# Kernel optimization log

Hardware: AMD Instinct MI355X
Metric: run time of the kernel (lower is better)

Reference implementation:

```python
import jax, jax.numpy as jnp
import numpy as np

SCALE = 2
BN_EPS = 1e-5


def setup_inputs() -> dict:
    key = jax.random.key(0)
    ks = jax.random.split(key, 12)
    B, C, H, W = 16, 256, 64, 64
    inter = C // 32  # reduce_ratio_nl = 32 -> 8
    f = lambda k, shape, s=0.05: jax.random.normal(k, shape, dtype=jnp.float32) * s
    return {
        "x": jax.random.normal(ks[0], (B, C, H, W), dtype=jnp.float32),
        "Wq": f(ks[1], (inter, C)), "bq": f(ks[2], (inter,)),
        "Wk": f(ks[3], (inter, C)), "bk": f(ks[4], (inter,)),
        "Wv": f(ks[5], (C, C)),    "bv": f(ks[6], (C,)),
        "gamma_nl": f(ks[7], (1,), 0.5),
        "convW": f(ks[8], (C, C, 3, 3)), "convb": f(ks[9], (C,)),
        "bn_w": jnp.ones((C,), jnp.float32),
        "bn_b": jnp.zeros((C,), jnp.float32),
        "bn_mean": f(ks[10], (C,)),
        "bn_var": jnp.ones((C,), jnp.float32),
        "gamma": f(ks[11], (1,), 0.5),
    }


def reference(x, Wq, bq, Wk, bk, Wv, bv, gamma_nl, convW, convb,
              bn_w, bn_b, bn_mean, bn_var, gamma):
    B, C, H, W = x.shape
    s = SCALE
    hb, wb = H // s, W // s
    L = hb * wb
    # split into s*s spatial blocks, batch them: [s*s*B, C, L]
    xb = (x.reshape(B, C, s, hb, s, wb)
           .transpose(2, 4, 0, 1, 3, 5)
           .reshape(s * s * B, C, L))
    # 1x1 conv projections == channel matmuls
    q = jnp.einsum('dc,ncl->ndl', Wq, xb) + bq[:, None]   # [N, d, L]
    k = jnp.einsum('dc,ncl->ndl', Wk, xb) + bk[:, None]
    v = jnp.einsum('dc,ncl->ndl', Wv, xb) + bv[:, None]   # [N, C, L]
    # energy[n,l,m] = sum_d q[n,d,l] * k[n,d,m]; softmax over last axis
    attn = jax.nn.softmax(jnp.einsum('ndl,ndm->nlm', q, k), axis=-1)
    # out[n,c,i] = sum_j v[n,c,j] * attn[n,i,j]
    out = jnp.einsum('ncj,nij->nci', v, attn)
    out = gamma_nl * out + xb
    # reassemble blocks -> [B, C, H, W]
    ctx = (out.reshape(s, s, B, C, hb, wb)
              .transpose(2, 3, 0, 4, 1, 5)
              .reshape(B, C, H, W))
    # 3x3 conv + BN (eval) + gamma-residual + ReLU
    y = jax.lax.conv_general_dilated(
        ctx, convW, window_strides=(1, 1), padding='SAME',
        dimension_numbers=('NCHW', 'OIHW', 'NCHW')) + convb[None, :, None, None]
    inv = (bn_w / jnp.sqrt(bn_var + BN_EPS))[None, :, None, None]
    y = (y - bn_mean[None, :, None, None]) * inv + bn_b[None, :, None, None]
    return jax.nn.relu(gamma * y + x)
```

## Files before the change

### kernel.cpp

```cpp
#include <hip/hip_runtime.h>
#include <hip/hip_bf16.h>
#include <math.h>

#define B_   16
#define C_   256
#define H_   64
#define W_   64
#define L_   1024
#define N_   64
#define D_   8

typedef _Float16 f16x8 __attribute__((ext_vector_type(8)));
typedef float    f32x4 __attribute__((ext_vector_type(4)));

static __device__ __forceinline__ unsigned short f16bits(float v) {
    _Float16 h = (_Float16)v;
    return *reinterpret_cast<unsigned short*>(&h);
}
static __device__ __forceinline__ float f16tof(unsigned short b) {
    _Float16 h = *reinterpret_cast<_Float16*>(&b);
    return (float)h;
}

__global__ __launch_bounds__(256) void qk_proj(
    const float* __restrict__ x, const float* __restrict__ Wq,
    const float* __restrict__ bq, const float* __restrict__ Wk,
    const float* __restrict__ bk, float* __restrict__ q, float* __restrict__ k)
{
    __shared__ float Ws[16][C_];
    __shared__ float bs[16];
    int t = threadIdx.x;
    for (int i = t; i < 8 * C_; i += 256) {
        Ws[i >> 8][i & 255]       = Wq[i];
        Ws[8 + (i >> 8)][i & 255] = Wk[i];
    }
    if (t < 8) { bs[t] = bq[t]; bs[8 + t] = bk[t]; }
    __syncthreads();

    int gid = blockIdx.x * 256 + t;
    int n = gid >> 10, l = gid & 1023;
    int si = n >> 5, sj = (n >> 4) & 1, b = n & 15;
    int h = si * 32 + (l >> 5), w = sj * 32 + (l & 31);
    const float* xp = x + ((size_t)(b * C_) * H_ + h) * W_ + w;

    float acc[16];
    #pragma unroll
    for (int d = 0; d < 16; d++) acc[d] = bs[d];

    for (int c0 = 0; c0 < C_; c0 += 4) {
        float xv[4];
        #pragma unroll
        for (int u = 0; u < 4; u++) xv[u] = xp[(size_t)(c0 + u) * (H_ * W_)];
        #pragma unroll
        for (int d = 0; d < 16; d++) {
            float4 wv = *reinterpret_cast<const float4*>(&Ws[d][c0]);
            acc[d] += wv.x * xv[0] + wv.y * xv[1] + wv.z * xv[2] + wv.w * xv[3];
        }
    }
    #pragma unroll
    for (int d = 0; d < 8; d++) q[((size_t)n * 8 + d) * L_ + l] = acc[d];
    #pragma unroll
    for (int d = 0; d < 8; d++) k[((size_t)n * 8 + d) * L_ + l] = acc[8 + d];
}

__global__ __launch_bounds__(256) void wprep2(
    const float* __restrict__ Wv, unsigned short* __restrict__ WV2)
{
    int e = blockIdx.x * 256 + threadIdx.x;
    int j  = e & 7;
    int l  = (e >> 3) & 63;
    int cf = (e >> 9) & 15;
    int kq = e >> 13;
    int c = cf * 16 + (l & 15);
    int k = kq * 32 + (l >> 4) * 8 + j;
    WV2[e] = f16bits(Wv[(size_t)c * C_ + k]);
}

__global__ __launch_bounds__(256, 2) void v_proj_mfma(
    const float* __restrict__ x, const unsigned short* __restrict__ WV2,
    const float* __restrict__ bv, unsigned short* __restrict__ vth)
{
    __shared__ __align__(16) unsigned short Xs[128][72];
    int bid = blockIdx.x;
    int n = bid >> 3, lt = bid & 7;
    int l0 = lt * 128;
    int si = n >> 5, sj = (n >> 4) & 1, b = n & 15;
    int t = threadIdx.x;
    int lane = t & 63, wv = t >> 6;
    int lane16 = lane & 15, lkg = lane >> 4;

    f32x4 acc[8][4];
    #pragma unroll
    for (int lf = 0; lf < 8; lf++)
        #pragma unroll
        for (int f = 0; f < 4; f++) acc[lf][f] = f32x4{0.f, 0.f, 0.f, 0.f};

    int hrow = si * 32 + (l0 >> 5) + wv;
    const float* xbase = x + ((size_t)b * C_) * (H_ * W_) + hrow * W_ + sj * 32;

    for (int kc = 0; kc < 4; kc++) {
        __syncthreads();
        const float* xp = xbase + (size_t)(kc * 64 + lane) * (H_ * W_);
        #pragma unroll
        for (int u4 = 0; u4 < 8; u4++) {
            float4 v = *reinterpret_cast<const float4*>(xp + u4 * 4);
            Xs[wv * 32 + u4 * 4 + 0][lane] = f16bits(v.x);
            Xs[wv * 32 + u4 * 4 + 1][lane] = f16bits(v.y);
            Xs[wv * 32 + u4 * 4 + 2][lane] = f16bits(v.z);
            Xs[wv * 32 + u4 * 4 + 3][lane] = f16bits(v.w);
        }
        __syncthreads();

        #pragma unroll
        for (int ks = 0; ks < 2; ks++) {
            int kq = kc * 2 + ks;
            f16x8 bh[4];
            #pragma unroll
            for (int f = 0; f < 4; f++) {
                size_t base = (((size_t)kq * 16 + (wv * 4 + f)) * 64 + lane) * 8;
                bh[f] = *reinterpret_cast<const f16x8*>(WV2 + base);
            }
            #pragma unroll
            for (int lf = 0; lf < 8; lf++) {
                f16x8 ah = *reinterpret_cast<const f16x8*>(
                    &Xs[lf * 16 + lane16][ks * 32 + lkg * 8]);
                #pragma unroll
                for (int f = 0; f < 4; f++)
                    acc[lf][f] = __builtin_amdgcn_mfma_f32_16x16x32_f16(ah, bh[f], acc[lf][f], 0, 0, 0);
            }
        }
    }

    float bias[4];
    #pragma unroll
    for (int f = 0; f < 4; f++) bias[f] = bv[(wv * 4 + f) * 16 + lane16];
    #pragma unroll
    for (int lf = 0; lf < 8; lf++) {
        #pragma unroll
        for (int f = 0; f < 4; f++) {
            int c = (wv * 4 + f) * 16 + lane16;
            unsigned short hb[4];
            #pragma unroll
            for (int e = 0; e < 4; e++)
                hb[e] = f16bits(acc[lf][f][e] + bias[f]);
            size_t base = ((size_t)n * C_ + c) * L_ + l0 + lf * 16 + lkg * 4;
            *reinterpret_cast<uint2*>(vth + base) = *reinterpret_cast<uint2*>(hb);
        }
    }
}

__global__ __launch_bounds__(256) void attn_mfma(
    const float* __restrict__ x, const float* __restrict__ q,
    const float* __restrict__ k, const unsigned short* __restrict__ vth,
    const float* __restrict__ gamma_nl_p, unsigned short* __restrict__ ctxh)
{
    int bid = blockIdx.x;
    int xcd = bid & 7, rr = bid >> 3;
    int n = (xcd << 3) | (rr >> 4);
    int it = rr & 15;
    int i0 = it * 64;
    int si = n >> 5, sj = (n >> 4) & 1, b = n & 15;

    __shared__ __align__(16) char smem[64 * 264 * 2];
    __shared__ float sums[64];
    char* Ph = smem;
    float (*Kt)[8][64] = (float (*)[8][64])(smem + 8192);
    float* scl = (float*)(smem + 8192 + 4096);

    int t = threadIdx.x;
    int l = t & 63, wv = t >> 6;
    int lane16 = l & 15, lkg = l >> 4;
    int srow = wv * 16 + (l >> 2);
    int sj4 = l & 3;

    float qr[8];
    #pragma unroll
    for (int d = 0; d < 8; d++)
        qr[d] = q[((size_t)n * 8 + d) * L_ + i0 + srow];

    #pragma unroll
    for (int u = 0; u < 2; u++) {
        int e = t + u * 256;
        int d = e >> 6, j = e & 63;
        Kt[0][d][j] = k[((size_t)n * 8 + d) * L_ + j];
    }

    float m = -1e30f, psum = 0.f;
    f32x4 acc[4][4];
    #pragma unroll
    for (int mf = 0; mf < 4; mf++)
        #pragma unroll
        for (int f = 0; f < 4; f++) acc[mf][f] = f32x4{0.f, 0.f, 0.f, 0.f};

    for (int tile = 0; tile < 16; tile++) {
        __syncthreads();
        int buf = tile & 1;

        float s[16];
        #pragma unroll
        for (int jj = 0; jj < 16; jj++) s[jj] = 0.f;
        #pragma unroll
        for (int d = 0; d < 8; d++) {
            const float* kp = &Kt[buf][d][sj4 * 16];
            float kv[16];
            *reinterpret_cast<float4*>(&kv[0])  = *reinterpret_cast<const float4*>(kp);
            *reinterpret_cast<float4*>(&kv[4])  = *reinterpret_cast<const float4*>(kp + 4);
            *reinterpret_cast<float4*>(&kv[8])  = *reinterpret_cast<const float4*>(kp + 8);
            *reinterpret_cast<float4*>(&kv[12]) = *reinterpret_cast<const float4*>(kp + 12);
            float qd = qr[d];
            #pragma unroll
            for (int jj = 0; jj < 16; jj++) s[jj] += qd * kv[jj];
        }

        float pmax = s[0];
        #pragma unroll
        for (int jj = 1; jj < 16; jj++) pmax = fmaxf(pmax, s[jj]);
        pmax = fmaxf(pmax, __shfl_xor(pmax, 1));
        pmax = fmaxf(pmax, __shfl_xor(pmax, 2));
        float mnew = fmaxf(m, pmax);
        float sc = __expf(m - mnew);
        m = mnew;
        psum *= sc;
        float p[16];
        #pragma unroll
        for (int jj = 0; jj < 16; jj++) {
            p[jj] = __expf(s[jj] - m);
            psum += p[jj];
        }
        if ((l & 3) == 0) scl[srow] = sc;

        #pragma unroll
        for (int g = 0; g < 2; g++) {
            unsigned short hb[8];
            #pragma unroll
            for (int u = 0; u < 8; u++) hb[u] = f16bits(p[g * 8 + u]);
            int jg = sj4 * 2 + g;
            int off = srow * 128 + ((jg ^ (srow & 7)) << 4);
            *reinterpret_cast<uint4*>(&Ph[off]) = *reinterpret_cast<uint4*>(hb);
        }
        __syncthreads();

        #pragma unroll
        for (int mf = 0; mf < 4; mf++) {
            #pragma unroll
            for (int e = 0; e < 4; e++) {
                float se = scl[mf * 16 + lkg * 4 + e];
                #pragma unroll
                for (int f = 0; f < 4; f++) acc[mf][f][e] *= se;
            }
        }

        if (tile < 15) {
            #pragma unroll
            for (int u = 0; u < 2; u++) {
                int e = t + u * 256;
                int d = e >> 6, j = e & 63;
                Kt[buf ^ 1][d][j] = k[((size_t)n * 8 + d) * L_ + (tile + 1) * 64 + j];
            }
        }

        int j0 = tile * 64;
        #pragma unroll
        for (int ks = 0; ks < 2; ks++) {
            f16x8 bh[4];
            #pragma unroll
            for (int f = 0; f < 4; f++) {
                size_t vbase = ((size_t)n * C_ + wv * 64 + f * 16 + lane16) * L_
                             + j0 + ks * 32 + lkg * 8;
                bh[f] = *reinterpret_cast<const f16x8*>(vth + vbase);
            }
            #pragma unroll
            for (int mf = 0; mf < 4; mf++) {
                int row = mf * 16 + lane16;
                int off = row * 128 + (((ks * 4 + lkg) ^ (row & 7)) << 4);
                f16x8 ah = *reinterpret_cast<const f16x8*>(&Ph[off]);
                #pragma unroll
                for (int f = 0; f < 4; f++)
                    acc[mf][f] = __builtin_amdgcn_mfma_f32_16x16x32_f16(ah, bh[f], acc[mf][f], 0, 0, 0);
            }
        }
    }

    psum += __shfl_xor(psum, 1);
    psum += __shfl_xor(psum, 2);
    if ((l & 3) == 0) sums[srow] = psum;
    __syncthreads();

    float g = gamma_nl_p[0];
    unsigned short* pool = (unsigned short*)smem;
    #pragma unroll
    for (int mf = 0; mf < 4; mf++) {
        #pragma unroll
        for (int e = 0; e < 4; e++) {
            int row = mf * 16 + lkg * 4 + e;
            int i = i0 + row;
            float rs = 1.0f / sums[row];
            int h = si * 32 + (i >> 5), w = sj * 32 + (i & 31);
            #pragma unroll
            for (int f = 0; f < 4; f++) {
                int c = wv * 64 + f * 16 + lane16;
                float xv = x[((size_t)(b * C_ + c)) * (H_ * W_) + (size_t)h * W_ + w];
                pool[row * 264 + c] = f16bits(g * (acc[mf][f][e] * rs) + xv);
            }
        }
    }
    __syncthreads();

    #pragma unroll
    for (int u = 0; u < 8; u++) {
        int chunk = t + u * 256;
        int row = chunk >> 5, cseg = (chunk & 31) * 8;
        int i = i0 + row;
        int h = si * 32 + (i >> 5), w = sj * 32 + (i & 31);
        size_t ci = (((size_t)b * H_ + h) * W_ + w) * C_ + cseg;
        *reinterpret_cast<uint4*>(&ctxh[ci]) =
            *reinterpret_cast<uint4*>(&pool[row * 264 + cseg]);
    }
}

__global__ __launch_bounds__(256) void wprep(
    const float* __restrict__ convW,
    unsigned short* __restrict__ WBh, unsigned short* __restrict__ WBl)
{
    int e = blockIdx.x * 256 + threadIdx.x;
    int j  = e & 7;
    int l  = (e >> 3) & 63;
    int cf = (e >> 9) & 15;
    int q  = (e >> 13) & 7;
    int tap = e >> 16;
    int co = cf * 16 + (l & 15);
    int ci = q * 32 + (l >> 4) * 8 + j;
    float v = convW[((size_t)co * C_ + ci) * 9 + tap];
    unsigned short hb = f16bits(v);
    WBh[e] = hb;
    WBl[e] = f16bits(v - f16tof(hb));
}

__global__ __launch_bounds__(256, 2) void conv_mfma(
    const unsigned short* __restrict__ ctxh,
    const unsigned short* __restrict__ WBh, const unsigned short* __restrict__ WBl,
    const float* __restrict__ convb, const float* __restrict__ bn_w,
    const float* __restrict__ bn_b, const float* __restrict__ bn_mean,
    const float* __restrict__ bn_var, const float* __restrict__ gamma_p,
    const float* __restrict__ x, float* __restrict__ out)
{
    __shared__ __align__(16) char Cs[1056 * 16];
    int t = threadIdx.x;
    int l = t & 63, wv = t >> 6;
    int lrow = l & 15, lkg = l >> 4;
    int b = blockIdx.x >> 5;
    int h0 = (blockIdx.x & 31) * 2;

    float gmm = gamma_p[0];
    float sA[4], sB[4];
    #pragma unroll
    for (int f = 0; f < 4; f++) {
        int co = wv * 64 + f * 16 + lrow;
        float inv = bn_w[co] * rsqrtf(bn_var[co] + 1e-5f);
        sA[f] = gmm * inv;
        sB[f] = gmm * ((convb[co] - bn_mean[co]) * inv + bn_b[co]);
    }

    f32x4 acc[8][4];
    #pragma unroll
    for (int mf = 0; mf < 8; mf++)
        #pragma unroll
        for (int f = 0; f < 4; f++) acc[mf][f] = f32x4{0.f, 0.f, 0.f, 0.f};

    for (int q = 0; q < 8; q++) {
        int ci0 = q * 32;
        __syncthreads();
        for (int idx = t; idx < 1056; idx += 256) {
            int kgp = idx & 3;
            int rem = idx >> 2;
            int wslot = rem % 66, hh = rem / 66;
            int h = h0 - 1 + hh, w = wslot - 1;
            int kg = kgp ^ ((wslot >> 1) & 3);
            uint4 v = uint4{0u, 0u, 0u, 0u};
            if ((unsigned)h < 64u && (unsigned)w < 64u)
                v = *reinterpret_cast<const uint4*>(
                    ctxh + ((((size_t)b * H_ + h) * W_ + w) * C_ + ci0 + kg * 8));
            *reinterpret_cast<uint4*>(&Cs[(rem * 4 + kgp) * 16]) = v;
        }
        __syncthreads();

        #pragma unroll
        for (int tap = 0; tap < 9; tap++) {
            const int kh = tap / 3, kw = tap % 3;
            f16x8 bh[4], bl[4];
            #pragma unroll
            for (int f = 0; f < 4; f++) {
                size_t base = ((((size_t)tap * 8 + q) * 16 + (wv * 4 + f)) * 64 + l) * 8;
                bh[f] = *reinterpret_cast<const f16x8*>(WBh + base);
                bl[f] = *reinterpret_cast<const f16x8*>(WBl + base);
            }
            #pragma unroll
            for (int mf = 0; mf < 8; mf++) {
                int wsl = (mf & 3) * 16 + lrow + kw;
                int hh = (mf >> 2) + kh;
                int kgp = lkg ^ ((wsl >> 1) & 3);
                int off = ((hh * 66 + wsl) * 4 + kgp) * 16;
                f16x8 ah = *reinterpret_cast<const f16x8*>(&Cs[off]);
                #pragma unroll
                for (int f = 0; f < 4; f++) {
                    acc[mf][f] = __builtin_amdgcn_mfma_f32_16x16x32_f16(ah, bh[f], acc[mf][f], 0, 0, 0);
                    acc[mf][f] = __builtin_amdgcn_mfma_f32_16x16x32_f16(ah, bl[f], acc[mf][f], 0, 0, 0);
                }
            }
        }
    }

    #pragma unroll
    for (int mf = 0; mf < 8; mf++) {
        int h = h0 + (mf >> 2);
        int wb = (mf & 3) * 16 + lkg * 4;
        #pragma unroll
        for (int f = 0; f < 4; f++) {
            int co = wv * 64 + f * 16 + lrow;
            size_t adr = (((size_t)b * C_ + co) * H_ + h) * W_ + wb;
            float4 xr = *reinterpret_cast<const float4*>(x + adr);
            float4 o;
            o.x = fmaxf(sA[f] * acc[mf][f][0] + sB[f] + xr.x, 0.f);
            o.y = fmaxf(sA[f] * acc[mf][f][1] + sB[f] + xr.y, 0.f);
            o.z = fmaxf(sA[f] * acc[mf][f][2] + sB[f] + xr.z, 0.f);
            o.w = fmaxf(sA[f] * acc[mf][f][3] + sB[f] + xr.w, 0.f);
            *reinterpret_cast<float4*>(out + adr) = o;
        }
    }
}

extern "C" void kernel_launch(void* const* d_in, const int* in_sizes, int n_in,
                              void* d_out, int out_size, void* d_ws, size_t ws_size,
                              hipStream_t stream)
{
    const float* x        = (const float*)d_in[0];
    const float* Wq       = (const float*)d_in[1];
    const float* bq       = (const float*)d_in[2];
    const float* Wk       = (const float*)d_in[3];
    const float* bk       = (const float*)d_in[4];
    const float* Wv       = (const float*)d_in[5];
    const float* bv       = (const float*)d_in[6];
    const float* gamma_nl = (const float*)d_in[7];
    const float* convW    = (const float*)d_in[8];
    const float* convb    = (const float*)d_in[9];
    const float* bn_w     = (const float*)d_in[10];
    const float* bn_b     = (const float*)d_in[11];
    const float* bn_mean  = (const float*)d_in[12];
    const float* bn_var   = (const float*)d_in[13];
    const float* gamma    = (const float*)d_in[14];
    float* out = (float*)d_out;

    float* q   = (float*)d_ws;
    float* k   = q  + (size_t)N_ * 8 * L_;
    unsigned short* vth  = (unsigned short*)(k + (size_t)N_ * 8 * L_);
    unsigned short* ctxh = vth + (size_t)N_ * C_ * L_;
    unsigned short* WBh  = ctxh + (size_t)B_ * C_ * H_ * W_;
    unsigned short* WBl  = WBh + (size_t)9 * 8 * 16 * 64 * 8;
    unsigned short* WV2  = WBl + (size_t)9 * 8 * 16 * 64 * 8;

    wprep<<<dim3(589824 / 256), dim3(256), 0, stream>>>(convW, WBh, WBl);
    wprep2<<<dim3(65536 / 256), dim3(256), 0, stream>>>(Wv, WV2);
    qk_proj<<<dim3(N_ * L_ / 256), dim3(256), 0, stream>>>(x, Wq, bq, Wk, bk, q, k);
    v_proj_mfma<<<dim3(512), dim3(256), 0, stream>>>(x, WV2, bv, vth);
    attn_mfma<<<dim3(1024), dim3(256), 0, stream>>>(
        x, q, k, vth, gamma_nl, ctxh);
    conv_mfma<<<dim3(512), dim3(256), 0, stream>>>(
        ctxh, WBh, WBl, convb, bn_w, bn_b, bn_mean, bn_var, gamma, x, out);
}
```

Before: 531.4 us.

## Drop split-fp16 conv weight correction and double-buffer input staging in conv

Removes the low-order fp16 residual weight copy, so the 3x3 conv runs one MFMA per fragment instead of two, halving its matrix work and weight traffic. It also double-buffers the shared-memory input tile, prefetching the next channel chunk into registers while the current chunk is computed, with one barrier per iteration. The cost is reduced precision in the conv weights, which now carry a single fp16 rounding, and more register and LDS use.

```diff
diff --git a/kernel.cpp b/kernel.cpp
--- a/kernel.cpp
+++ b/kernel.cpp
@@ -16,10 +16,6 @@
 static __device__ __forceinline__ unsigned short f16bits(float v) {
     _Float16 h = (_Float16)v;
     return *reinterpret_cast<unsigned short*>(&h);
-}
-static __device__ __forceinline__ float f16tof(unsigned short b) {
-    _Float16 h = *reinterpret_cast<_Float16*>(&b);
-    return (float)h;
 }
 
 __global__ __launch_bounds__(256) void qk_proj(
@@ -319,8 +315,7 @@
 }
 
 __global__ __launch_bounds__(256) void wprep(
-    const float* __restrict__ convW,
-    unsigned short* __restrict__ WBh, unsigned short* __restrict__ WBl)
+    const float* __restrict__ convW, unsigned short* __restrict__ WBh)
 {
     int e = blockIdx.x * 256 + threadIdx.x;
     int j  = e & 7;
@@ -330,21 +325,18 @@
     int tap = e >> 16;
     int co = cf * 16 + (l & 15);
     int ci = q * 32 + (l >> 4) * 8 + j;
-    float v = convW[((size_t)co * C_ + ci) * 9 + tap];
-    unsigned short hb = f16bits(v);
-    WBh[e] = hb;
-    WBl[e] = f16bits(v - f16tof(hb));
+    WBh[e] = f16bits(convW[((size_t)co * C_ + ci) * 9 + tap]);
 }
 
 __global__ __launch_bounds__(256, 2) void conv_mfma(
     const unsigned short* __restrict__ ctxh,
-    const unsigned short* __restrict__ WBh, const unsigned short* __restrict__ WBl,
+    const unsigned short* __restrict__ WBh,
     const float* __restrict__ convb, const float* __restrict__ bn_w,
     const float* __restrict__ bn_b, const float* __restrict__ bn_mean,
     const float* __restrict__ bn_var, const float* __restrict__ gamma_p,
     const float* __restrict__ x, float* __restrict__ out)
 {
-    __shared__ __align__(16) char Cs[1056 * 16];
+    __shared__ __align__(16) uint4 Cs[2][1056];
     int t = threadIdx.x;
     int l = t & 63, wv = t >> 6;
     int lrow = l & 15, lkg = l >> 4;
@@ -367,10 +359,11 @@
         #pragma unroll
         for (int f = 0; f < 4; f++) acc[mf][f] = f32x4{0.f, 0.f, 0.f, 0.f};
 
-    for (int q = 0; q < 8; q++) {
+    auto ldq = [&](int q, uint4* rv) {
         int ci0 = q * 32;
-        __syncthreads();
-        for (int idx = t; idx < 1056; idx += 256) {
+        #pragma unroll
+        for (int u = 0; u < 4; u++) {
+            int idx = t + u * 256;
             int kgp = idx & 3;
             int rem = idx >> 2;
             int wslot = rem % 66, hh = rem / 66;
@@ -380,34 +373,62 @@
             if ((unsigned)h < 64u && (unsigned)w < 64u)
                 v = *reinterpret_cast<const uint4*>(
                     ctxh + ((((size_t)b * H_ + h) * W_ + w) * C_ + ci0 + kg * 8));
-            *reinterpret_cast<uint4*>(&Cs[(rem * 4 + kgp) * 16]) = v;
-        }
-        __syncthreads();
+            rv[u] = v;
+        }
+        rv[4] = uint4{0u, 0u, 0u, 0u};
+        if (t < 32) {
+            int idx = t + 1024;
+            int kgp = idx & 3;
+            int rem = idx >> 2;
+            int wslot = rem % 66, hh = rem / 66;
+            int h = h0 - 1 + hh, w = wslot - 1;
+            int kg = kgp ^ ((wslot >> 1) & 3);
+            if ((unsigned)h < 64u && (unsigned)w < 64u)
+                rv[4] = *reinterpret_cast<const uint4*>(
+                    ctxh + ((((size_t)b * H_ + h) * W_ + w) * C_ + ci0 + kg * 8));
+        }
+    };
+    auto wrq = [&](int buf, const uint4* rv) {
+        #pragma unroll
+        for (int u = 0; u < 4; u++) Cs[buf][t + u * 256] = rv[u];
+        if (t < 32) Cs[buf][t + 1024] = rv[4];
+    };
+
+    {
+        uint4 rv[5];
+        ldq(0, rv);
+        wrq(0, rv);
+    }
+    __syncthreads();
+
+    for (int q = 0; q < 8; q++) {
+        int cur = q & 1;
+        uint4 rnext[5];
+        if (q < 7) ldq(q + 1, rnext);
 
         #pragma unroll
         for (int tap = 0; tap < 9; tap++) {
             const int kh = tap / 3, kw = tap % 3;
-            f16x8 bh[4], bl[4];
+            f16x8 bh[4];
             #pragma unroll
             for (int f = 0; f < 4; f++) {
                 size_t base = ((((size_t)tap * 8 + q) * 16 + (wv * 4 + f)) * 64 + l) * 8;
                 bh[f] = *reinterpret_cast<const f16x8*>(WBh + base);
-                bl[f] = *reinterpret_cast<const f16x8*>(WBl + base);
             }
             #pragma unroll
             for (int mf = 0; mf < 8; mf++) {
                 int wsl = (mf & 3) * 16 + lrow + kw;
                 int hh = (mf >> 2) + kh;
                 int kgp = lkg ^ ((wsl >> 1) & 3);
-                int off = ((hh * 66 + wsl) * 4 + kgp) * 16;
-                f16x8 ah = *reinterpret_cast<const f16x8*>(&Cs[off]);
+                f16x8 ah = *reinterpret_cast<const f16x8*>(&Cs[cur][(hh * 66 + wsl) * 4 + kgp]);
                 #pragma unroll
-                for (int f = 0; f < 4; f++) {
+                for (int f = 0; f < 4; f++)
                     acc[mf][f] = __builtin_amdgcn_mfma_f32_16x16x32_f16(ah, bh[f], acc[mf][f], 0, 0, 0);
-                    acc[mf][f] = __builtin_amdgcn_mfma_f32_16x16x32_f16(ah, bl[f], acc[mf][f], 0, 0, 0);
-                }
-            }
-        }
+            }
+        }
+
+        if (q < 7) wrq(cur ^ 1, rnext);
+        __syncthreads();
     }
 
     #pragma unroll
@@ -455,15 +476,14 @@
     unsigned short* vth  = (unsigned short*)(k + (size_t)N_ * 8 * L_);
     unsigned short* ctxh = vth + (size_t)N_ * C_ * L_;
     unsigned short* WBh  = ctxh + (size_t)B_ * C_ * H_ * W_;
-    unsigned short* WBl  = WBh + (size_t)9 * 8 * 16 * 64 * 8;
-    unsigned short* WV2  = WBl + (size_t)9 * 8 * 16 * 64 * 8;
-
-    wprep<<<dim3(589824 / 256), dim3(256), 0, stream>>>(convW, WBh, WBl);
+    unsigned short* WV2  = WBh + (size_t)9 * 8 * 16 * 64 * 8;
+
+    wprep<<<dim3(589824 / 256), dim3(256), 0, stream>>>(convW, WBh);
     wprep2<<<dim3(65536 / 256), dim3(256), 0, stream>>>(Wv, WV2);
     qk_proj<<<dim3(N_ * L_ / 256), dim3(256), 0, stream>>>(x, Wq, bq, Wk, bk, q, k);
     v_proj_mfma<<<dim3(512), dim3(256), 0, stream>>>(x, WV2, bv, vth);
     attn_mfma<<<dim3(1024), dim3(256), 0, stream>>>(
         x, q, k, vth, gamma_nl, ctxh);
     conv_mfma<<<dim3(512), dim3(256), 0, stream>>>(
-        ctxh, WBh, WBl, convb, bn_w, bn_b, bn_mean, bn_var, gamma, x, out);
-}
+        ctxh, WBh, convb, bn_w, bn_b, bn_mean, bn_var, gamma, x, out);
+}
```

Result: slower. 611.8 us (+15.1%).
